# Performance work log

Hardware: AMD Instinct MI355X
Metric: run time of the kernel (lower is better)

The kernel has to match this reference:

```python
import jax, jax.numpy as jnp
import numpy as np

# Problem sizes (production-scale detection head)
B, N, C = 8, 10000, 80
K = 8           # max_output_size_per_class
MAX_TOTAL = 8   # max_total_size
IOU_THR = 0.5
SCORE_THR = 0.5
NEG = -1e9      # large-negative sentinel for suppressed / below-threshold scores


def setup_inputs() -> dict:
    key = jax.random.key(0)
    k1, k2 = jax.random.split(key)
    boxes = jax.random.uniform(k1, (B, N, 1, 4), dtype=jnp.float32)   # [y1,x1,y2,x2] in [0,1)
    scores = jax.random.uniform(k2, (B, N, C), dtype=jnp.float32)
    return {"boxes": boxes, "scores": scores}


def _iou_one_vs_all(b, boxes):
    # b: [4], boxes: [N,4]; standard IoU (same formula TF NMS uses, no reordering)
    y1, x1, y2, x2 = b[0], b[1], b[2], b[3]
    Y1, X1, Y2, X2 = boxes[:, 0], boxes[:, 1], boxes[:, 2], boxes[:, 3]
    ih = jnp.maximum(jnp.minimum(y2, Y2) - jnp.maximum(y1, Y1), 0.0)
    iw = jnp.maximum(jnp.minimum(x2, X2) - jnp.maximum(x1, X1), 0.0)
    inter = ih * iw
    area = (y2 - y1) * (x2 - x1)
    areas = (Y2 - Y1) * (X2 - X1)
    union = area + areas - inter
    return inter / jnp.maximum(union, 1e-9)


def _nms_single(boxes, scores):
    # Greedy NMS for one (batch, class): boxes [N,4], scores [N] -> K selections.
    s0 = jnp.where(scores > SCORE_THR, scores, NEG)

    def step(s, _):
        idx = jnp.argmax(s)
        sc = s[idx]
        valid = sc > SCORE_THR  # masked entries are NEG, so this == above-threshold
        b = boxes[idx]
        iou = _iou_one_vs_all(b, boxes)            # [N]
        s = jnp.where(iou > IOU_THR, NEG, s)       # suppress overlapping boxes
        s = s.at[idx].set(NEG)                     # remove the selected box itself
        return s, (idx, sc, valid, b)

    _, (idxs, scs, valids, bsel) = jax.lax.scan(step, s0, None, length=K)
    return idxs, scs, valids, bsel  # [K], [K], [K], [K,4]


def _combined_nms(boxes, scores):
    # boxes [B,N,4] (class-agnostic, q=1), scores [B,N,C]
    scores_cn = jnp.transpose(scores, (0, 2, 1))  # [B,C,N]
    per_class = jax.vmap(lambda bx, sc: jax.vmap(lambda s: _nms_single(bx, s))(sc))
    idxs, scs, valids, bsel = per_class(boxes, scores_cn)  # [B,C,K], bsel [B,C,K,4]

    # Combine across classes: global top MAX_TOTAL by score (pad_per_class=False)
    masked = jnp.where(valids, scs, NEG).reshape(B, C * K)
    top_sc, top_idx = jax.lax.top_k(masked, MAX_TOTAL)     # [B,T]
    classes = (top_idx // K).astype(jnp.int32)             # candidate class id
    bflat = bsel.reshape(B, C * K, 4)
    vflat = valids.reshape(B, C * K)
    top_boxes = jnp.take_along_axis(bflat, top_idx[..., None], axis=1)  # [B,T,4]
    top_valid = jnp.take_along_axis(vflat, top_idx, axis=1)             # [B,T]

    out_boxes = jnp.where(top_valid[..., None], jnp.clip(top_boxes, 0.0, 1.0), 0.0)  # clip_boxes=True
    out_scores = jnp.where(top_valid, top_sc, 0.0)
    out_classes = jnp.where(top_valid, classes, 0)
    valid_det = jnp.sum(top_valid, axis=1).astype(jnp.int32)
    return out_boxes, out_scores, out_classes, valid_det


def reference(boxes, scores):
    # boxes: [B,N,1,4], scores: [B,N,C]
    return _combined_nms(boxes[:, :, 0, :], scores)
```

## Files before the change

kernel.cpp:

```cpp
#include <hip/hip_runtime.h>
#include <math.h>

#define BATCH 8
#define NBOX 10000
#define NCLS 80
#define KSEL 8
#define MAXT 8
#define IOU_THR 0.5f
#define SCORE_THR 0.5f
#define NEGV -1000000000.0f
#define IDXINF 0x7fffffff

#define NSUB 80
#define CHROWS 640
typedef unsigned long long u64;

__device__ __forceinline__ u64 pk20(float v, int n) {
    return ((u64)__float_as_uint(v) << 20) | ((u64)(16383 - n) << 6);
}

#define T2C(V1, I1, V2, I2, X, N)                                           \
    do {                                                                    \
        float _x = ((X) > SCORE_THR) ? (X) : NEGV;                          \
        if (_x > (V1)) { (V2)=(V1); (I2)=(I1); (V1)=_x; (I1)=(N); }         \
        else if (_x > (V2)) { (V2)=_x; (I2)=(N); }                          \
    } while (0)

#define INS4(T1, T2, T3, T4, K)                                             \
    do { u64 _k = (K);                                                      \
        if (_k > (T1)) { (T4)=(T3); (T3)=(T2); (T2)=(T1); (T1)=_k; }        \
        else if (_k > (T2)) { (T4)=(T3); (T3)=(T2); (T2)=_k; }              \
        else if (_k > (T3)) { (T4)=(T3); (T3)=_k; }                         \
        else if (_k > (T4)) { (T4)=_k; }                                    \
    } while (0)

#define IOU_SUP(KB, KA)                                                     \
    do {                                                                    \
        float ih = fmaxf(__fsub_rn(fminf((KB).z, cb.z), fmaxf((KB).x, cb.x)), 0.0f); \
        float iw = fmaxf(__fsub_rn(fminf((KB).w, cb.w), fmaxf((KB).y, cb.y)), 0.0f); \
        float inter = __fmul_rn(ih, iw);                                    \
        float uni   = __fsub_rn(__fadd_rn((KA), carea), inter);             \
        float iou   = __fdiv_rn(inter, fmaxf(uni, 1e-9f));                  \
        if (iou > IOU_THR) sup = true;                                      \
    } while (0)

__device__ __forceinline__ float aload(const float* p) {
    return __hip_atomic_load(p, __ATOMIC_RELAXED, __HIP_MEMORY_SCOPE_AGENT);
}

__global__ __launch_bounds__(320) void class_heads(
    const float* __restrict__ scores,
    u64* __restrict__ hk,
    int* __restrict__ cnt)
{
    __shared__ u64 lk[16][NCLS][2];

    const int bid = blockIdx.x;
    const int b   = bid & 7;
    const int sub = bid >> 3;
    const int n0  = sub * 128;
    const int tid = threadIdx.x;
    const int q   = tid % 20;
    const int g   = tid / 20;

    if (bid == 0 && tid < BATCH) cnt[tid] = 0;

    const float* base = scores + ((size_t)b * NBOX + n0) * NCLS + 4 * q;

    float v10 = NEGV, v20 = NEGV, v11 = NEGV, v21 = NEGV;
    float v12 = NEGV, v22 = NEGV, v13 = NEGV, v23 = NEGV;
    int   i10 = IDXINF, i20 = IDXINF, i11 = IDXINF, i21 = IDXINF;
    int   i12 = IDXINF, i22 = IDXINF, i13 = IDXINF, i23 = IDXINF;

    #pragma unroll
    for (int k = 0; k < 8; ++k) {
        const int n = n0 + g * 8 + k;
        if (n < NBOX) {
            float4 x = *(const float4*)(base + (size_t)(g * 8 + k) * NCLS);
            T2C(v10, i10, v20, i20, x.x, n);
            T2C(v11, i11, v21, i21, x.y, n);
            T2C(v12, i12, v22, i22, x.z, n);
            T2C(v13, i13, v23, i23, x.w, n);
        }
    }

    const int c0 = 4 * q;
    lk[g][c0 + 0][0] = (v10 > SCORE_THR) ? pk20(v10, i10) : 0;
    lk[g][c0 + 0][1] = (v20 > SCORE_THR) ? pk20(v20, i20) : 0;
    lk[g][c0 + 1][0] = (v11 > SCORE_THR) ? pk20(v11, i11) : 0;
    lk[g][c0 + 1][1] = (v21 > SCORE_THR) ? pk20(v21, i21) : 0;
    lk[g][c0 + 2][0] = (v12 > SCORE_THR) ? pk20(v12, i12) : 0;
    lk[g][c0 + 2][1] = (v22 > SCORE_THR) ? pk20(v22, i22) : 0;
    lk[g][c0 + 3][0] = (v13 > SCORE_THR) ? pk20(v13, i13) : 0;
    lk[g][c0 + 3][1] = (v23 > SCORE_THR) ? pk20(v23, i23) : 0;
    __syncthreads();

    if (tid < NCLS) {
        u64 h1 = 0, h2 = 0;
        #pragma unroll
        for (int g2 = 0; g2 < 16; ++g2) {
            u64 a1 = lk[g2][tid][0], a2 = lk[g2][tid][1];
            if (a1 > h1) { u64 t = h1; h1 = a1; h2 = (a2 > t) ? a2 : t; }
            else if (a1 > h2) h2 = a1;
        }
        u64* o = hk + ((size_t)(b * NCLS + tid) * NSUB + sub) * 2;
        o[0] = h1; o[1] = h2;
    }
}

__global__ __launch_bounds__(256) void chunk_heads(
    const u64* __restrict__ hk,
    u64* __restrict__ sk8)
{
    __shared__ u64 keys[8][20];

    const int bc  = blockIdx.x;
    const int tid = threadIdx.x;
    if (tid < 160) keys[tid / 20][tid % 20] = hk[(size_t)bc * 160 + tid];
    __syncthreads();

    const int ch  = tid >> 5;
    const int l32 = tid & 31;

    const u64 mykey = (l32 < 20) ? keys[ch][l32] : 0;
    int rank = 0, nnz = 0;
    #pragma unroll
    for (int i = 0; i < 20; ++i) {
        const u64 ki = keys[ch][i];
        rank += (ki > mykey) ? 1 : 0;
        nnz  += (ki != 0) ? 1 : 0;
    }
    u64* o = sk8 + (size_t)bc * 64 + ch * 8;
    if (mykey != 0 && rank < 8) o[rank] = mykey;
    const int fill = (nnz < 8) ? nnz : 8;
    if (l32 >= fill && l32 < 8) o[l32] = 0;
}

__global__ __launch_bounds__(256) void nms_extract(
    const u64* __restrict__ hk,
    const u64* __restrict__ sk8,
    const float* __restrict__ scores,
    const float* __restrict__ boxes,
    float* __restrict__ ws_msc,
    float* __restrict__ ws_box,
    int*   __restrict__ cnt,
    float* __restrict__ out)
{
    __shared__ u64    kds[4][64];
    __shared__ float4 bds[4][64];
    __shared__ int    lut[4][64];
    __shared__ float  rv[2][4];
    __shared__ int    ri[2][4];
    __shared__ int    s_old;

    const int bid = blockIdx.x;
    const int b   = bid & 7;
    const int grp = bid >> 3;
    const int w   = threadIdx.x >> 6;
    const int l   = threadIdx.x & 63;
    const int tid = threadIdx.x;
    const int c   = grp * 4 + w;
    const int bc  = b * NCLS + c;

    const float*  raw  = scores + (size_t)b * NBOX * NCLS + c;
    const float4* box4 = (const float4*)(boxes + (size_t)b * NBOX * 4);

    const int r8 = l & 7;

    const u64 k = sk8[(size_t)bc * 64 + l];

    float4 bx = make_float4(0.f, 0.f, 0.f, 0.f);
    float  oa = 0.f;
    if (k) {
        const int n = 16383 - (int)((k >> 6) & 0x3FFF);
        bx = box4[n];
        oa = __fmul_rn(__fsub_rn(bx.z, bx.x), __fsub_rn(bx.w, bx.y));
    }

    kds[w][l] = k;
    bds[w][l] = bx;
    int rank = 0;
    {
        const ulonglong2* kp = (const ulonglong2*)kds[w];
        #pragma unroll
        for (int j = 0; j < 32; ++j) {
            ulonglong2 t = kp[j];
            rank += (t.x > k) ? 1 : 0;
            rank += (t.y > k) ? 1 : 0;
        }
    }
    if (k) lut[w][rank] = l;
    const int live = __popcll(__ballot(k != 0));

    int  kept = 0;
    u64  term = 0;
    bool sup  = false;
    u64    sk  = 0;
    float4 sbx = make_float4(0.f, 0.f, 0.f, 0.f);
    for (int r = 0; r < live; ++r) {
        const int cand = lut[w][r];
        const u64 smask = __ballot(sup);
        if (!((smask >> cand) & 1)) {
            const float4 kb = bds[w][cand];
            const float kba = __fmul_rn(__fsub_rn(kb.z, kb.x),
                                        __fsub_rn(kb.w, kb.y));
            {
                float ih = fmaxf(__fsub_rn(fminf(kb.z, bx.z), fmaxf(kb.x, bx.x)), 0.0f);
                float iw = fmaxf(__fsub_rn(fminf(kb.w, bx.w), fmaxf(kb.y, bx.y)), 0.0f);
                float inter = __fmul_rn(ih, iw);
                float uni   = __fsub_rn(__fadd_rn(kba, oa), inter);
                float iou   = __fdiv_rn(inter, fmaxf(uni, 1e-9f));
                if (iou > IOU_THR) sup = true;
            }
            if (l == kept) { sk = kds[w][cand]; sbx = kb; }
            kept++;
            if (kept == MAXT) { term = kds[w][cand]; break; }
        }
    }

    const u64 bad = __ballot((r8 == 7) && (k != 0) && (k > term));

    if (!bad) {
        if (l < kept) {
            const int o = bc * KSEL + l;
            ws_msc[o] = __uint_as_float((unsigned)(sk >> 20));
            float* ob = ws_box + (size_t)o * 4;
            ob[0] = sbx.x; ob[1] = sbx.y; ob[2] = sbx.z; ob[3] = sbx.w;
        } else if (l < MAXT) {
            const int o = bc * KSEL + l;
            ws_msc[o] = NEGV;
            float* ob = ws_box + (size_t)o * 4;
            ob[0] = 0.f; ob[1] = 0.f; ob[2] = 0.f; ob[3] = 0.f;
        }
    } else {
        const int ch = l >> 2;
        const int r4 = l & 3;
        u64 k4 = 0;
        {
            u64 t1 = 0, t2 = 0, t3 = 0, t4 = 0;
            const u64* hp = hk + ((size_t)bc * NSUB + ch * 5) * 2;
            #pragma unroll
            for (int j = 0; j < 10; ++j) INS4(t1, t2, t3, t4, hp[j]);
            k4 = (r4 == 0) ? t1 : (r4 == 1) ? t2 : (r4 == 2) ? t3 : t4;
        }
        float4 fbx = make_float4(0.f, 0.f, 0.f, 0.f);
        float  fba = 0.f;
        if (k4) {
            const int n = 16383 - (int)((k4 >> 6) & 0x3FFF);
            fbx = box4[n];
            fba = __fmul_rn(__fsub_rn(fbx.z, fbx.x), __fsub_rn(fbx.w, fbx.y));
        }
        u64  fkey = k4 ? (k4 | (u64)l) : 0;
        bool dead = (fkey == 0);
        const u64 zb = __ballot(k4 == 0);
        bool exh  = (zb >> (l | 3)) & 1;
        u64  fl   = 0;

        float4 kb0, kb1, kb2, kb3, kb4, kb5, kb6, kb7;
        float  ka0=0, ka1=0, ka2=0, ka3=0, ka4=0, ka5=0, ka6=0, ka7=0;
        kb0 = kb1 = kb2 = kb3 = kb4 = kb5 = kb6 = kb7 = make_float4(0, 0, 0, 0);
        kept = 0;

        for (;;) {
            u64 lk_ = dead ? 0ull : fkey;
            #pragma unroll
            for (int off = 1; off < 64; off <<= 1) {
                u64 o = __shfl_xor(lk_, off, 64);
                if (o > lk_) lk_ = o;
            }
            const u64 db = __ballot(dead);
            const bool blind = (((db >> (l & ~3)) & 15ull) == 15ull)
                             && (fl != 0) && !exh;
            if (__any(blind)) {
                u64 fk = blind ? fl : 0ull;
                #pragma unroll
                for (int off = 1; off < 64; off <<= 1) {
                    u64 o = __shfl_xor(fk, off, 64);
                    if (o > fk) fk = o;
                }
                if (fk > lk_) {
                    const int chr = ((int)(fk & 63ull)) >> 2;
                    const u64 flc = fk & ~63ull;
                    const int nb  = chr * CHROWS;
                    u64 s1 = 0, s2 = 0, s3 = 0, s4 = 0;
                    #pragma unroll
                    for (int qq = 0; qq < 10; ++qq) {
                        const int n = nb + qq * 64 + l;
                        if (n < NBOX) {
                            float x = raw[(size_t)n * NCLS];
                            if (x > SCORE_THR) {
                                u64 kx = pk20(x, n);
                                if (kx < flc) INS4(s1, s2, s3, s4, kx);
                            }
                        }
                    }
                    #pragma unroll
                    for (int off = 1; off < 64; off <<= 1) {
                        u64 o1 = __shfl_xor(s1, off, 64);
                        u64 o2 = __shfl_xor(s2, off, 64);
                        u64 o3 = __shfl_xor(s3, off, 64);
                        u64 o4 = __shfl_xor(s4, off, 64);
                        INS4(s1, s2, s3, s4, o1); INS4(s1, s2, s3, s4, o2);
                        INS4(s1, s2, s3, s4, o3); INS4(s1, s2, s3, s4, o4);
                    }
                    if (ch == chr) {
                        u64 t = (r4 == 0) ? s1 : (r4 == 1) ? s2
                              : (r4 == 2) ? s3 : s4;
                        exh  = (s4 == 0);
                        fkey = t ? (t | (u64)l) : 0;
                        dead = (fkey == 0);
                        fl   = 0;
                        if (!dead) {
                            const int n = 16383 - (int)((fkey >> 6) & 0x3FFF);
                            fbx = box4[n];
                            fba = __fmul_rn(__fsub_rn(fbx.z, fbx.x),
                                            __fsub_rn(fbx.w, fbx.y));
                        }
                    }
                    continue;
                }
            }
            if (lk_ == 0ull) break;

            const int   owner = (int)(lk_ & 63ull);
            const float bv    = __uint_as_float((unsigned)(lk_ >> 20));
            float4 cb;
            cb.x = __shfl(fbx.x, owner, 64);
            cb.y = __shfl(fbx.y, owner, 64);
            cb.z = __shfl(fbx.z, owner, 64);
            cb.w = __shfl(fbx.w, owner, 64);
            const float carea = __shfl(fba, owner, 64);

            bool sup2 = false;
            {
                bool sup = false;
                if (kept > 0) IOU_SUP(kb0, ka0);
                if (kept > 1) IOU_SUP(kb1, ka1);
                if (kept > 2) IOU_SUP(kb2, ka2);
                if (kept > 3) IOU_SUP(kb3, ka3);
                if (kept > 4) IOU_SUP(kb4, ka4);
                if (kept > 5) IOU_SUP(kb5, ka5);
                if (kept > 6) IOU_SUP(kb6, ka6);
                if (kept > 7) IOU_SUP(kb7, ka7);
                sup2 = sup;
            }

            if (!sup2) {
                if (l == 0) {
                    const int o = bc * KSEL + kept;
                    ws_msc[o] = bv;
                    float* ob = ws_box + (size_t)o * 4;
                    ob[0] = cb.x; ob[1] = cb.y; ob[2] = cb.z; ob[3] = cb.w;
                }
                if      (kept == 0) { kb0 = cb; ka0 = carea; }
                else if (kept == 1) { kb1 = cb; ka1 = carea; }
                else if (kept == 2) { kb2 = cb; ka2 = carea; }
                else if (kept == 3) { kb3 = cb; ka3 = carea; }
                else if (kept == 4) { kb4 = cb; ka4 = carea; }
                else if (kept == 5) { kb5 = cb; ka5 = carea; }
                else if (kept == 6) { kb6 = cb; ka6 = carea; }
                else                { kb7 = cb; ka7 = carea; }
                kept++;
            }

            if (l == owner) dead = true;
            if (ch == (owner >> 2) && !exh) fl = lk_;
            if (kept == MAXT) break;
        }

        if (l == 0) {
            for (int k2 = kept; k2 < MAXT; ++k2) {
                const int o = bc * KSEL + k2;
                ws_msc[o] = NEGV;
                float* ob = ws_box + (size_t)o * 4;
                ob[0] = 0.f; ob[1] = 0.f; ob[2] = 0.f; ob[3] = 0.f;
            }
        }
    }

    __syncthreads();
    if (tid == 0) {
        __threadfence();
        s_old = atomicAdd(&cnt[b], 1);
    }
    __syncthreads();
    if (s_old != (NCLS / 4) - 1) return;
    __threadfence();

    const float* msc = ws_msc + b * NCLS * KSEL;
    float v0 = aload(msc + tid);
    float v1 = aload(msc + tid + 256);
    float v2 = (tid + 512 < NCLS * KSEL) ? aload(msc + tid + 512) : -INFINITY;

    const int OFF_SC = BATCH * MAXT * 4;
    const int OFF_CL = OFF_SC + BATCH * MAXT;
    const int OFF_VD = OFF_CL + BATCH * MAXT;

    int tot = 0;
    int p = 0;
    #pragma unroll
    for (int t = 0; t < MAXT; ++t) {
        float bv = v0; int bi = tid;
        if (v1 > bv) { bv = v1; bi = tid + 256; }
        if (v2 > bv) { bv = v2; bi = tid + 512; }
        #pragma unroll
        for (int off = 32; off > 0; off >>= 1) {
            float ov = __shfl_down(bv, off, 64);
            int   oi = __shfl_down(bi, off, 64);
            if (ov > bv || (ov == bv && oi < bi)) { bv = ov; bi = oi; }
        }
        if ((tid & 63) == 0) { rv[p][tid >> 6] = bv; ri[p][tid >> 6] = bi; }
        __syncthreads();
        bv = rv[p][0]; bi = ri[p][0];
        #pragma unroll
        for (int w2 = 1; w2 < 4; ++w2) {
            float ov = rv[p][w2]; int oi = ri[p][w2];
            if (ov > bv || (ov == bv && oi < bi)) { bv = ov; bi = oi; }
        }
        p ^= 1;

        const bool valid = bv > SCORE_THR;
        tot += valid ? 1 : 0;
        if (tid == t) {
            const float* sb = ws_box + ((size_t)b * NCLS * KSEL + bi) * 4;
            float bx0 = aload(sb + 0), bx1 = aload(sb + 1);
            float bx2 = aload(sb + 2), bx3 = aload(sb + 3);
            float* ob = out + ((size_t)b * MAXT + t) * 4;
            ob[0] = valid ? fminf(fmaxf(bx0, 0.0f), 1.0f) : 0.0f;
            ob[1] = valid ? fminf(fmaxf(bx1, 0.0f), 1.0f) : 0.0f;
            ob[2] = valid ? fminf(fmaxf(bx2, 0.0f), 1.0f) : 0.0f;
            ob[3] = valid ? fminf(fmaxf(bx3, 0.0f), 1.0f) : 0.0f;
            out[OFF_SC + b * MAXT + t] = valid ? bv : 0.0f;
            out[OFF_CL + b * MAXT + t] = valid ? (float)(bi >> 3) : 0.0f;
        }
        if (tid == (bi & 255)) {
            int w2 = bi >> 8;
            if (w2 == 0) v0 = -INFINITY;
            else if (w2 == 1) v1 = -INFINITY;
            else v2 = -INFINITY;
        }
    }
    if (tid == 0) out[OFF_VD + b] = (float)tot;
}

extern "C" void kernel_launch(void* const* d_in, const int* in_sizes, int n_in,
                              void* d_out, int out_size, void* d_ws, size_t ws_size,
                              hipStream_t stream) {
    const float* boxes  = (const float*)d_in[0];
    const float* scores = (const float*)d_in[1];
    float* out = (float*)d_out;

    const size_t nk = (size_t)BATCH * NCLS * NSUB * 2;
    char* p = (char*)d_ws;
    u64*   hk     = (u64*)p;          p += nk * 8;
    u64*   sk8    = (u64*)p;          p += (size_t)BATCH * NCLS * 64 * 8;
    float* ws_msc = (float*)p;        p += (size_t)BATCH * NCLS * KSEL * 4;
    float* ws_box = (float*)p;        p += (size_t)BATCH * NCLS * KSEL * 16;
    int*   cnt    = (int*)p;

    class_heads<<<BATCH * NSUB, 320, 0, stream>>>(scores, hk, cnt);
    chunk_heads<<<BATCH * NCLS, 256, 0, stream>>>(hk, sk8);
    nms_extract<<<BATCH * (NCLS / 4), 256, 0, stream>>>(hk, sk8, scores, boxes,
                                                        ws_msc, ws_box,
                                                        cnt, out);
}
```

Before: 31.90 us.

## Precompute pairwise IoU suppression bitmasks and prefetch candidate boxes earlier

The greedy NMS loop over up to 64 candidates used to compute IoU against each kept box one by one, with a ballot and a divide on every serial step. Now each lane sorts itself by rank, computes a 64-bit suppression mask against all higher-ranked candidates in one unrolled pass, and the greedy selection then runs as cheap bitmask operations with ffs and ballot. Box gathers for the candidates move into chunk_heads, which writes them to a new workspace buffer, so the extract kernel reads contiguous float4s instead of doing dependent random loads. The cost is 64 IoU computations per lane where fewer serial ones were needed before, plus extra workspace traffic.

```diff
diff --git a/kernel.cpp b/kernel.cpp
--- a/kernel.cpp
+++ b/kernel.cpp
@@ -110,17 +110,21 @@
 
 __global__ __launch_bounds__(256) void chunk_heads(
     const u64* __restrict__ hk,
-    u64* __restrict__ sk8)
+    const float* __restrict__ boxes,
+    u64* __restrict__ sk8,
+    float4* __restrict__ sbx)
 {
     __shared__ u64 keys[8][20];
 
     const int bc  = blockIdx.x;
+    const int b   = bc / NCLS;
     const int tid = threadIdx.x;
     if (tid < 160) keys[tid / 20][tid % 20] = hk[(size_t)bc * 160 + tid];
     __syncthreads();
 
     const int ch  = tid >> 5;
     const int l32 = tid & 31;
+    const float4* box4 = (const float4*)(boxes + (size_t)b * NBOX * 4);
 
     const u64 mykey = (l32 < 20) ? keys[ch][l32] : 0;
     int rank = 0, nnz = 0;
@@ -130,15 +134,23 @@
         rank += (ki > mykey) ? 1 : 0;
         nnz  += (ki != 0) ? 1 : 0;
     }
-    u64* o = sk8 + (size_t)bc * 64 + ch * 8;
-    if (mykey != 0 && rank < 8) o[rank] = mykey;
+    u64*    o  = sk8 + (size_t)bc * 64 + ch * 8;
+    float4* ob = sbx + (size_t)bc * 64 + ch * 8;
+    if (mykey != 0 && rank < 8) {
+        o[rank]  = mykey;
+        ob[rank] = box4[16383 - (int)((mykey >> 6) & 0x3FFF)];
+    }
     const int fill = (nnz < 8) ? nnz : 8;
-    if (l32 >= fill && l32 < 8) o[l32] = 0;
+    if (l32 >= fill && l32 < 8) {
+        o[l32]  = 0;
+        ob[l32] = make_float4(0.f, 0.f, 0.f, 0.f);
+    }
 }
 
 __global__ __launch_bounds__(256) void nms_extract(
     const u64* __restrict__ hk,
     const u64* __restrict__ sk8,
+    const float4* __restrict__ sbx,
     const float* __restrict__ scores,
     const float* __restrict__ boxes,
     float* __restrict__ ws_msc,
@@ -149,6 +161,8 @@
     __shared__ u64    kds[4][64];
     __shared__ float4 bds[4][64];
     __shared__ int    lut[4][64];
+    __shared__ u64    kr[4][64];
+    __shared__ float4 br[4][64];
     __shared__ float  rv[2][4];
     __shared__ int    ri[2][4];
     __shared__ int    s_old;
@@ -167,15 +181,8 @@
 
     const int r8 = l & 7;
 
-    const u64 k = sk8[(size_t)bc * 64 + l];
-
-    float4 bx = make_float4(0.f, 0.f, 0.f, 0.f);
-    float  oa = 0.f;
-    if (k) {
-        const int n = 16383 - (int)((k >> 6) & 0x3FFF);
-        bx = box4[n];
-        oa = __fmul_rn(__fsub_rn(bx.z, bx.x), __fsub_rn(bx.w, bx.y));
-    }
+    const u64    k  = sk8[(size_t)bc * 64 + l];
+    const float4 bx = sbx[(size_t)bc * 64 + l];
 
     kds[w][l] = k;
     bds[w][l] = bx;
@@ -192,41 +199,59 @@
     if (k) lut[w][rank] = l;
     const int live = __popcll(__ballot(k != 0));
 
-    int  kept = 0;
-    u64  term = 0;
-    bool sup  = false;
-    u64    sk  = 0;
-    float4 sbx = make_float4(0.f, 0.f, 0.f, 0.f);
-    for (int r = 0; r < live; ++r) {
-        const int cand = lut[w][r];
-        const u64 smask = __ballot(sup);
-        if (!((smask >> cand) & 1)) {
-            const float4 kb = bds[w][cand];
+    u64    rk = 0;
+    float4 rb = make_float4(0.f, 0.f, 0.f, 0.f);
+    if (l < live) {
+        const int src = lut[w][l];
+        rk = kds[w][src];
+        rb = bds[w][src];
+    }
+    kr[w][l] = rk;
+    br[w][l] = rb;
+    const float ra = __fmul_rn(__fsub_rn(rb.z, rb.x), __fsub_rn(rb.w, rb.y));
+
+    u64 mymask = 0;
+    {
+        const float4* bp = br[w];
+        #pragma unroll
+        for (int j = 0; j < 64; ++j) {
+            const float4 kb = bp[j];
             const float kba = __fmul_rn(__fsub_rn(kb.z, kb.x),
                                         __fsub_rn(kb.w, kb.y));
-            {
-                float ih = fmaxf(__fsub_rn(fminf(kb.z, bx.z), fmaxf(kb.x, bx.x)), 0.0f);
-                float iw = fmaxf(__fsub_rn(fminf(kb.w, bx.w), fmaxf(kb.y, bx.y)), 0.0f);
-                float inter = __fmul_rn(ih, iw);
-                float uni   = __fsub_rn(__fadd_rn(kba, oa), inter);
-                float iou   = __fdiv_rn(inter, fmaxf(uni, 1e-9f));
-                if (iou > IOU_THR) sup = true;
-            }
-            if (l == kept) { sk = kds[w][cand]; sbx = kb; }
-            kept++;
-            if (kept == MAXT) { term = kds[w][cand]; break; }
-        }
-    }
+            float ih = fmaxf(__fsub_rn(fminf(kb.z, rb.z), fmaxf(kb.x, rb.x)), 0.0f);
+            float iw = fmaxf(__fsub_rn(fminf(kb.w, rb.w), fmaxf(kb.y, rb.y)), 0.0f);
+            float inter = __fmul_rn(ih, iw);
+            float uni   = __fsub_rn(__fadd_rn(kba, ra), inter);
+            float iou   = __fdiv_rn(inter, fmaxf(uni, 1e-9f));
+            if (j < l && iou > IOU_THR) mymask |= 1ull << j;
+        }
+    }
+
+    u64 alive = (live >= 64) ? ~0ull : ((1ull << live) - 1ull);
+    u64 kept8 = 0;
+    int cnt8  = 0;
+    int lastr = 0;
+    while (alive) {
+        const int r = __ffsll((long long)alive) - 1;
+        kept8 |= 1ull << r;
+        lastr = r;
+        alive &= ~(1ull << r);
+        if (++cnt8 == MAXT) break;
+        alive &= ~__ballot((mymask >> r) & 1);
+    }
+    const u64 term = (cnt8 == MAXT) ? kr[w][lastr] : 0;
 
     const u64 bad = __ballot((r8 == 7) && (k != 0) && (k > term));
 
     if (!bad) {
-        if (l < kept) {
-            const int o = bc * KSEL + l;
-            ws_msc[o] = __uint_as_float((unsigned)(sk >> 20));
+        if ((kept8 >> l) & 1) {
+            const int slot = (int)__popcll(kept8 & ((1ull << l) - 1ull));
+            const int o = bc * KSEL + slot;
+            ws_msc[o] = __uint_as_float((unsigned)(rk >> 20));
             float* ob = ws_box + (size_t)o * 4;
-            ob[0] = sbx.x; ob[1] = sbx.y; ob[2] = sbx.z; ob[3] = sbx.w;
-        } else if (l < MAXT) {
+            ob[0] = rb.x; ob[1] = rb.y; ob[2] = rb.z; ob[3] = rb.w;
+        }
+        if (l >= cnt8 && l < MAXT) {
             const int o = bc * KSEL + l;
             ws_msc[o] = NEGV;
             float* ob = ws_box + (size_t)o * 4;
@@ -259,7 +284,7 @@
         float4 kb0, kb1, kb2, kb3, kb4, kb5, kb6, kb7;
         float  ka0=0, ka1=0, ka2=0, ka3=0, ka4=0, ka5=0, ka6=0, ka7=0;
         kb0 = kb1 = kb2 = kb3 = kb4 = kb5 = kb6 = kb7 = make_float4(0, 0, 0, 0);
-        kept = 0;
+        int kept = 0;
 
         for (;;) {
             u64 lk_ = dead ? 0ull : fkey;
@@ -452,15 +477,16 @@
 
     const size_t nk = (size_t)BATCH * NCLS * NSUB * 2;
     char* p = (char*)d_ws;
-    u64*   hk     = (u64*)p;          p += nk * 8;
-    u64*   sk8    = (u64*)p;          p += (size_t)BATCH * NCLS * 64 * 8;
-    float* ws_msc = (float*)p;        p += (size_t)BATCH * NCLS * KSEL * 4;
-    float* ws_box = (float*)p;        p += (size_t)BATCH * NCLS * KSEL * 16;
-    int*   cnt    = (int*)p;
+    u64*    hk     = (u64*)p;         p += nk * 8;
+    u64*    sk8    = (u64*)p;         p += (size_t)BATCH * NCLS * 64 * 8;
+    float4* sbx    = (float4*)p;      p += (size_t)BATCH * NCLS * 64 * 16;
+    float*  ws_msc = (float*)p;       p += (size_t)BATCH * NCLS * KSEL * 4;
+    float*  ws_box = (float*)p;       p += (size_t)BATCH * NCLS * KSEL * 16;
+    int*    cnt    = (int*)p;
 
     class_heads<<<BATCH * NSUB, 320, 0, stream>>>(scores, hk, cnt);
-    chunk_heads<<<BATCH * NCLS, 256, 0, stream>>>(hk, sk8);
-    nms_extract<<<BATCH * (NCLS / 4), 256, 0, stream>>>(hk, sk8, scores, boxes,
-                                                        ws_msc, ws_box,
+    chunk_heads<<<BATCH * NCLS, 256, 0, stream>>>(hk, boxes, sk8, sbx);
+    nms_extract<<<BATCH * (NCLS / 4), 256, 0, stream>>>(hk, sk8, sbx, scores,
+                                                        boxes, ws_msc, ws_box,
                                                         cnt, out);
 }
```

New measurement: 37.14 us. +16.4%, slower.

## Fuse chunk head selection into NMS extract kernel via shared memory

Applied to the files above, without the earlier changes.

Removes the separate chunk_heads kernel. Each wavefront of nms_extract now loads its class's 160 head keys into shared memory and ranks them per chunk to build the top-8-per-chunk key list locally. The fallback path also reads those keys from shared memory instead of global memory. This saves a kernel launch and the sk8 global round trip, at the cost of more LDS use and extra ranking work per block. The code relies on wavefront-synchronous LDS ordering with no barrier.

```diff
diff --git a/kernel.cpp b/kernel.cpp
--- a/kernel.cpp
+++ b/kernel.cpp
@@ -108,37 +108,8 @@
     }
 }
 
-__global__ __launch_bounds__(256) void chunk_heads(
-    const u64* __restrict__ hk,
-    u64* __restrict__ sk8)
-{
-    __shared__ u64 keys[8][20];
-
-    const int bc  = blockIdx.x;
-    const int tid = threadIdx.x;
-    if (tid < 160) keys[tid / 20][tid % 20] = hk[(size_t)bc * 160 + tid];
-    __syncthreads();
-
-    const int ch  = tid >> 5;
-    const int l32 = tid & 31;
-
-    const u64 mykey = (l32 < 20) ? keys[ch][l32] : 0;
-    int rank = 0, nnz = 0;
-    #pragma unroll
-    for (int i = 0; i < 20; ++i) {
-        const u64 ki = keys[ch][i];
-        rank += (ki > mykey) ? 1 : 0;
-        nnz  += (ki != 0) ? 1 : 0;
-    }
-    u64* o = sk8 + (size_t)bc * 64 + ch * 8;
-    if (mykey != 0 && rank < 8) o[rank] = mykey;
-    const int fill = (nnz < 8) ? nnz : 8;
-    if (l32 >= fill && l32 < 8) o[l32] = 0;
-}
-
 __global__ __launch_bounds__(256) void nms_extract(
     const u64* __restrict__ hk,
-    const u64* __restrict__ sk8,
     const float* __restrict__ scores,
     const float* __restrict__ boxes,
     float* __restrict__ ws_msc,
@@ -146,6 +117,7 @@
     int*   __restrict__ cnt,
     float* __restrict__ out)
 {
+    __shared__ u64    hkey[4][160];
     __shared__ u64    kds[4][64];
     __shared__ float4 bds[4][64];
     __shared__ int    lut[4][64];
@@ -167,17 +139,33 @@
 
     const int r8 = l & 7;
 
-    const u64 k = sk8[(size_t)bc * 64 + l];
-
+    {
+        const u64* hp = hk + (size_t)bc * 160;
+        hkey[w][l]       = hp[l];
+        hkey[w][l + 64]  = hp[l + 64];
+        if (l < 32) hkey[w][l + 128] = hp[l + 128];
+        kds[w][l] = 0;
+    }
+
+    #pragma unroll
+    for (int t = 0; t < 3; ++t) {
+        const int i = l + t * 64;
+        if (i < 160) {
+            const u64 key = hkey[w][i];
+            const int ch  = i / 20;
+            const u64* kp = &hkey[w][ch * 20];
+            int rank = 0;
+            #pragma unroll
+            for (int j = 0; j < 20; ++j)
+                rank += (kp[j] > key) ? 1 : 0;
+            if (key != 0 && rank < 8) kds[w][ch * 8 + rank] = key;
+        }
+    }
+
+    const u64 k = kds[w][l];
     float4 bx = make_float4(0.f, 0.f, 0.f, 0.f);
-    float  oa = 0.f;
-    if (k) {
-        const int n = 16383 - (int)((k >> 6) & 0x3FFF);
-        bx = box4[n];
-        oa = __fmul_rn(__fsub_rn(bx.z, bx.x), __fsub_rn(bx.w, bx.y));
-    }
-
-    kds[w][l] = k;
+    if (k) bx = box4[16383 - (int)((k >> 6) & 0x3FFF)];
+
     bds[w][l] = bx;
     int rank = 0;
     {
@@ -191,6 +179,7 @@
     }
     if (k) lut[w][rank] = l;
     const int live = __popcll(__ballot(k != 0));
+    const float oa = __fmul_rn(__fsub_rn(bx.z, bx.x), __fsub_rn(bx.w, bx.y));
 
     int  kept = 0;
     u64  term = 0;
@@ -238,7 +227,7 @@
         u64 k4 = 0;
         {
             u64 t1 = 0, t2 = 0, t3 = 0, t4 = 0;
-            const u64* hp = hk + ((size_t)bc * NSUB + ch * 5) * 2;
+            const u64* hp = &hkey[w][ch * 10];
             #pragma unroll
             for (int j = 0; j < 10; ++j) INS4(t1, t2, t3, t4, hp[j]);
             k4 = (r4 == 0) ? t1 : (r4 == 1) ? t2 : (r4 == 2) ? t3 : t4;
@@ -453,14 +442,12 @@
     const size_t nk = (size_t)BATCH * NCLS * NSUB * 2;
     char* p = (char*)d_ws;
     u64*   hk     = (u64*)p;          p += nk * 8;
-    u64*   sk8    = (u64*)p;          p += (size_t)BATCH * NCLS * 64 * 8;
     float* ws_msc = (float*)p;        p += (size_t)BATCH * NCLS * KSEL * 4;
     float* ws_box = (float*)p;        p += (size_t)BATCH * NCLS * KSEL * 16;
     int*   cnt    = (int*)p;
 
     class_heads<<<BATCH * NSUB, 320, 0, stream>>>(scores, hk, cnt);
-    chunk_heads<<<BATCH * NCLS, 256, 0, stream>>>(hk, sk8);
-    nms_extract<<<BATCH * (NCLS / 4), 256, 0, stream>>>(hk, sk8, scores, boxes,
+    nms_extract<<<BATCH * (NCLS / 4), 256, 0, stream>>>(hk, scores, boxes,
                                                         ws_msc, ws_box,
                                                         cnt, out);
 }
```

Result: faster. 29.32 us, median of 2 (-8.1%).
